# Performance work log

Hardware: AMD Instinct MI355X
Metric: run time of the kernel (lower is better)

Reference implementation:

```python
import jax, jax.numpy as jnp
import numpy as np

B, C, H, W, O = 32, 512, 28, 28, 1024


def _make_sketch(key, input_dim, output_dim):
    kh, ks = jax.random.split(key)
    rand_h = jax.random.randint(kh, (input_dim,), 0, output_dim)
    rand_s = jax.random.randint(ks, (input_dim,), 0, 2).astype(jnp.float32) * 2.0 - 1.0
    sketch = jnp.zeros((output_dim, input_dim), dtype=jnp.float32)
    return sketch.at[rand_h, jnp.arange(input_dim)].set(rand_s)


def setup_inputs() -> dict:
    key = jax.random.key(0)
    k1, k2, k3, k4 = jax.random.split(key, 4)
    x1 = jax.random.normal(k1, (B, C, H, W), dtype=jnp.float32)
    x2 = jax.random.normal(k2, (B, C, H, W), dtype=jnp.float32)
    sketch1 = _make_sketch(k3, C, O)
    sketch2 = _make_sketch(k4, C, O)
    return {"x1": x1, "x2": x2, "sketch1": sketch1, "sketch2": sketch2}


def reference(x1, x2, sketch1, sketch2):
    b, c, h, w = x1.shape
    out_dim = sketch1.shape[0]
    # [B, C, H*W] -> [B, N, C]
    x1_flat = x1.reshape(b, c, h * w).transpose(0, 2, 1)
    x2_flat = x2.reshape(b, c, h * w).transpose(0, 2, 1)
    # count-sketch projection via dense matmul (faithful to F.linear)
    proj1 = jnp.einsum('bnc,oc->bno', x1_flat, sketch1)
    proj2 = jnp.einsum('bnc,oc->bno', x2_flat, sketch2)
    orig_dtype = proj1.dtype
    # circular convolution via FFT along output_dim axis
    fft1 = jnp.fft.fft(proj1.astype(jnp.float32), axis=-1)
    fft2 = jnp.fft.fft(proj2.astype(jnp.float32), axis=-1)
    cbp_flat = jnp.fft.ifft(fft1 * fft2, axis=-1).real.astype(orig_dtype)
    # [B, N, O] -> [B, O, H, W]
    return cbp_flat.transpose(0, 2, 1).reshape(b, out_dim, h, w)
```

## Files before the change

kernel.cpp:

```cpp
#include <hip/hip_runtime.h>

#define O_DIM   1024
#define C_DIM   512
#define HW      784
#define B_DIM   32
#define T_POS   8
#define NTILES  (HW / T_POS)
#define NTHREADS 256

typedef float v2f __attribute__((ext_vector_type(2)));

__device__ __forceinline__ v2f cmul(v2f a, v2f b) {
    v2f bs = __builtin_shufflevector(b, b, 1, 0);
    v2f an = {-a.y, a.y};
    return a.x * b + an * bs;
}

static constexpr int REV5[32] = {
    0,16,8,24,4,20,12,28,2,18,10,26,6,22,14,30,
    1,17,9,25,5,21,13,29,3,19,11,27,7,23,15,31};

static constexpr float C32T[16] = {
    1.f, 0.98078528f, 0.92387953f, 0.83146961f,
    0.70710678f, 0.55557023f, 0.38268343f, 0.19509032f,
    0.f, -0.19509032f, -0.38268343f, -0.55557023f,
    -0.70710678f, -0.83146961f, -0.92387953f, -0.98078528f};
static constexpr float S32T[16] = {
    0.f, 0.19509032f, 0.38268343f, 0.55557023f,
    0.70710678f, 0.83146961f, 0.92387953f, 0.98078528f,
    1.f, 0.98078528f, 0.92387953f, 0.83146961f,
    0.70710678f, 0.55557023f, 0.38268343f, 0.19509032f};

__device__ __forceinline__ void fft32f(v2f y[32]) {
#pragma unroll
    for (int s = 0; s < 5; ++s) {
        const int L = 32 >> s;
        const int h = 16 >> s;
#pragma unroll
        for (int u = 0; u < 16; ++u) {
            const int blk = u >> (4 - s);
            const int t   = u & (h - 1);
            const int i   = blk * L + t;
            const int m   = t << s;
            v2f a = y[i], b = y[i + h];
            y[i] = a + b;
            v2f d = a - b;
            if (m == 0) {
                y[i + h] = d;
            } else if (m == 8) {
                y[i + h] = (v2f){d.y, -d.x};
            } else {
                y[i + h] = cmul(d, (v2f){C32T[m], -S32T[m]});
            }
        }
    }
}

__device__ __forceinline__ void four_step_Bf(v2f* zg, int p, v2f y[32]) {
    float sv, cv;
    __sincosf(-6.283185307179586f * (float)p * (1.f / 1024.f), &sv, &cv);
    const v2f stw = {cv, sv};
    v2f t2  = cmul(stw, stw);
    v2f t4  = cmul(t2, t2);
    v2f s8  = cmul(t4, t4);
    v2f s16 = cmul(s8, s8);
    v2f s24 = cmul(s16, s8);
    v2f wq0 = {1.f, 0.f}, wq1 = s8, wq2 = s16, wq3 = s24;
#pragma unroll
    for (int m = 0; m < 8; ++m) {
        {   const int k2 = m;
            v2f val = y[REV5[k2]];
            if (k2 > 0) val = cmul(val, wq0);
            zg[k2 * 32 + ((p + k2) & 31)] = val; }
        {   const int k2 = 8 + m;
            zg[k2 * 32 + ((p + k2) & 31)] = cmul(y[REV5[k2]], wq1); }
        {   const int k2 = 16 + m;
            zg[k2 * 32 + ((p + k2) & 31)] = cmul(y[REV5[k2]], wq2); }
        {   const int k2 = 24 + m;
            zg[k2 * 32 + ((p + k2) & 31)] = cmul(y[REV5[k2]], wq3); }
        if (m < 7) {
            wq0 = cmul(wq0, stw); wq1 = cmul(wq1, stw);
            wq2 = cmul(wq2, stw); wq3 = cmul(wq3, stw);
        }
    }
    __builtin_amdgcn_wave_barrier();
#pragma unroll
    for (int n1 = 0; n1 < 32; ++n1)
        y[n1] = zg[p * 32 + ((n1 + p) & 31)];
    __builtin_amdgcn_wave_barrier();
    fft32f(y);
}

__global__ void extract_sketch(const float* __restrict__ sk1,
                               const float* __restrict__ sk2,
                               int* __restrict__ h, float* __restrict__ s) {
    const int o = blockIdx.x;
    for (int c = threadIdx.x; c < C_DIM; c += blockDim.x) {
        float v1 = sk1[o * C_DIM + c];
        if (v1 != 0.f) { h[c] = o; s[c] = v1; }
        float v2 = sk2[o * C_DIM + c];
        if (v2 != 0.f) { h[C_DIM + c] = o; s[C_DIM + c] = v2; }
    }
}

__global__ __launch_bounds__(NTHREADS, 2)
void cbp_main(const float* __restrict__ x1, const float* __restrict__ x2,
              const int* __restrict__ h1, const int* __restrict__ h2,
              const float* __restrict__ s1, const float* __restrict__ s2,
              float* __restrict__ out) {
    __shared__ float4 LBUF[4096];
    float* Zs = reinterpret_cast<float*>(LBUF);
    float* R  = reinterpret_cast<float*>(LBUF);

    const int tid  = threadIdx.x;
    const int b    = blockIdx.x / NTILES;
    const int tile = blockIdx.x % NTILES;
    const int n0   = tile * T_POS;

    const int c0 = tid;
    const int c1 = tid + NTHREADS;
    const int xoff = b * (C_DIM * HW) + n0;
    const float4* p10 = (const float4*)(x1 + xoff + c0 * HW);
    const float4* p11 = (const float4*)(x1 + xoff + c1 * HW);
    const float4* p20 = (const float4*)(x2 + xoff + c0 * HW);
    const float4* p21 = (const float4*)(x2 + xoff + c1 * HW);
    float4 a0 = p10[0], a1 = p10[1];
    float4 b0 = p11[0], b1 = p11[1];
    float4 d0 = p20[0], d1 = p20[1];
    float4 e0 = p21[0], e1 = p21[1];
    const int   q10 = h1[c0], q11 = h1[c1], q20 = h2[c0], q21 = h2[c1];
    const float w10 = s1[c0], w11 = s1[c1], w20 = s2[c0], w21 = s2[c1];

#pragma unroll
    for (int i = 0; i < 4096 / NTHREADS; ++i)
        LBUF[tid + NTHREADS * i] = make_float4(0.f, 0.f, 0.f, 0.f);
    __syncthreads();

    {
        float v[8];
        v[0]=a0.x; v[1]=a0.y; v[2]=a0.z; v[3]=a0.w;
        v[4]=a1.x; v[5]=a1.y; v[6]=a1.z; v[7]=a1.w;
#pragma unroll
        for (int j = 0; j < 8; ++j)
            atomicAdd(&Zs[(j * O_DIM + q10) * 2 + 0], w10 * v[j]);
        v[0]=b0.x; v[1]=b0.y; v[2]=b0.z; v[3]=b0.w;
        v[4]=b1.x; v[5]=b1.y; v[6]=b1.z; v[7]=b1.w;
#pragma unroll
        for (int j = 0; j < 8; ++j)
            atomicAdd(&Zs[(j * O_DIM + q11) * 2 + 0], w11 * v[j]);
        v[0]=d0.x; v[1]=d0.y; v[2]=d0.z; v[3]=d0.w;
        v[4]=d1.x; v[5]=d1.y; v[6]=d1.z; v[7]=d1.w;
#pragma unroll
        for (int j = 0; j < 8; ++j)
            atomicAdd(&Zs[(j * O_DIM + q20) * 2 + 1], w20 * v[j]);
        v[0]=e0.x; v[1]=e0.y; v[2]=e0.z; v[3]=e0.w;
        v[4]=e1.x; v[5]=e1.y; v[6]=e1.z; v[7]=e1.w;
#pragma unroll
        for (int j = 0; j < 8; ++j)
            atomicAdd(&Zs[(j * O_DIM + q21) * 2 + 1], w21 * v[j]);
    }
    __syncthreads();

    const int g    = tid >> 5;
    const int p    = tid & 31;
    const int lane = tid & 63;
    v2f* zg = reinterpret_cast<v2f*>(LBUF) + g * O_DIM;
    const int paddr = (((lane & 32) | ((32 - p) & 31))) << 2;

    v2f y[32];

#pragma unroll 1
    for (int iter = 0; iter < 2; ++iter) {
        if (iter == 0) {
#pragma unroll
            for (int n2 = 0; n2 < 32; ++n2)
                y[n2] = zg[p + 32 * n2];
            __builtin_amdgcn_wave_barrier();
        } else {
            v2f t[32];
#pragma unroll
            for (int n2 = 0; n2 < 32; ++n2) {
                v2f za = y[REV5[n2]];
                v2f yb = y[REV5[31 - n2]];
                v2f zb;
                zb.x = __uint_as_float((unsigned)__builtin_amdgcn_ds_bpermute(
                           paddr, (int)__float_as_uint(yb.x)));
                zb.y = __uint_as_float((unsigned)__builtin_amdgcn_ds_bpermute(
                           paddr, (int)__float_as_uint(yb.y)));
                v2f self = y[REV5[(32 - n2) & 31]];
                zb.x = (p == 0) ? self.x : zb.x;
                zb.y = (p == 0) ? self.y : zb.y;
                v2f F1c = { za.x + zb.x, zb.y - za.y };
                v2f F2c = { za.y + zb.y, za.x - zb.x };
                t[n2] = cmul(F1c, F2c);
            }
#pragma unroll
            for (int i = 0; i < 32; ++i) y[i] = t[i];
        }
        fft32f(y);
        four_step_Bf(zg, p, y);
    }
    __syncthreads();

#pragma unroll
    for (int k1 = 0; k1 < 32; ++k1)
        R[(p + 32 * k1) * 10 + g] = y[REV5[k1]].x * (0.25f / 1024.f);
    __syncthreads();

    const int obase = b * (O_DIM * HW) + n0;
#pragma unroll
    for (int r = 0; r < O_DIM / NTHREADS; ++r) {
        const int o = tid + NTHREADS * r;
        const float* rp = &R[o * 10];
        float4 v0 = make_float4(rp[0], rp[1], rp[2], rp[3]);
        float4 v1 = make_float4(rp[4], rp[5], rp[6], rp[7]);
        float4* dst = (float4*)(out + obase + o * HW);
        dst[0] = v0;
        dst[1] = v1;
    }
}

extern "C" void kernel_launch(void* const* d_in, const int* in_sizes, int n_in,
                              void* d_out, int out_size, void* d_ws, size_t ws_size,
                              hipStream_t stream) {
    const float* x1  = (const float*)d_in[0];
    const float* x2  = (const float*)d_in[1];
    const float* sk1 = (const float*)d_in[2];
    const float* sk2 = (const float*)d_in[3];
    float* out = (float*)d_out;

    int*   h = (int*)d_ws;
    float* s = (float*)((char*)d_ws + 4096);

    hipLaunchKernelGGL(extract_sketch, dim3(O_DIM), dim3(256), 0, stream,
                       sk1, sk2, h, s);
    hipLaunchKernelGGL(cbp_main, dim3(B_DIM * NTILES), dim3(NTHREADS), 0, stream,
                       x1, x2, h, h + C_DIM, s, s + C_DIM, out);
}
```

Baseline: 359.6 us.

## Halve position tile per block, swizzle block-to-work mapping, use workgroup-scope LDS atomics

Each block now handles 4 spatial positions with 128 threads and half the LDS. That doubles the block count and should raise occupancy. Block IDs are remapped in a strided way, probably to spread neighbouring tiles across XCDs. The scatter atomics now use relaxed workgroup-scope fetch_add, and the output staging buffer uses a tighter pad. In exchange, each block writes only 16-byte segments per output row, which may hurt write coalescing, and each thread issues more x loads and atomics.

```diff
diff --git a/kernel.cpp b/kernel.cpp
--- a/kernel.cpp
+++ b/kernel.cpp
@@ -4,9 +4,11 @@
 #define C_DIM   512
 #define HW      784
 #define B_DIM   32
-#define T_POS   8
+#define T_POS   4
 #define NTILES  (HW / T_POS)
-#define NTHREADS 256
+#define NTHREADS 128
+#define NBLK    (B_DIM * NTILES)
+#define RPAD    5
 
 typedef float v2f __attribute__((ext_vector_type(2)));
 
@@ -108,56 +110,49 @@
               const int* __restrict__ h1, const int* __restrict__ h2,
               const float* __restrict__ s1, const float* __restrict__ s2,
               float* __restrict__ out) {
-    __shared__ float4 LBUF[4096];
+    __shared__ float4 LBUF[2048];
     float* Zs = reinterpret_cast<float*>(LBUF);
     float* R  = reinterpret_cast<float*>(LBUF);
 
-    const int tid  = threadIdx.x;
-    const int b    = blockIdx.x / NTILES;
-    const int tile = blockIdx.x % NTILES;
+    const int tid = threadIdx.x;
+    const int wid  = blockIdx.x;
+    const int work = (wid & 7) * (NBLK >> 3) + (wid >> 3);
+    const int b    = work / NTILES;
+    const int tile = work % NTILES;
     const int n0   = tile * T_POS;
 
-    const int c0 = tid;
-    const int c1 = tid + NTHREADS;
     const int xoff = b * (C_DIM * HW) + n0;
-    const float4* p10 = (const float4*)(x1 + xoff + c0 * HW);
-    const float4* p11 = (const float4*)(x1 + xoff + c1 * HW);
-    const float4* p20 = (const float4*)(x2 + xoff + c0 * HW);
-    const float4* p21 = (const float4*)(x2 + xoff + c1 * HW);
-    float4 a0 = p10[0], a1 = p10[1];
-    float4 b0 = p11[0], b1 = p11[1];
-    float4 d0 = p20[0], d1 = p20[1];
-    float4 e0 = p21[0], e1 = p21[1];
-    const int   q10 = h1[c0], q11 = h1[c1], q20 = h2[c0], q21 = h2[c1];
-    const float w10 = s1[c0], w11 = s1[c1], w20 = s2[c0], w21 = s2[c1];
-
-#pragma unroll
-    for (int i = 0; i < 4096 / NTHREADS; ++i)
+    float4 xa[4], xb[4];
+    int    qa[4], qb[4];
+    float  wa[4], wb[4];
+#pragma unroll
+    for (int r = 0; r < 4; ++r) {
+        const int c = tid + NTHREADS * r;
+        xa[r] = *(const float4*)(x1 + xoff + c * HW);
+        xb[r] = *(const float4*)(x2 + xoff + c * HW);
+        qa[r] = h1[c];  qb[r] = h2[c];
+        wa[r] = s1[c];  wb[r] = s2[c];
+    }
+
+#pragma unroll
+    for (int i = 0; i < 2048 / NTHREADS; ++i)
         LBUF[tid + NTHREADS * i] = make_float4(0.f, 0.f, 0.f, 0.f);
     __syncthreads();
 
-    {
-        float v[8];
-        v[0]=a0.x; v[1]=a0.y; v[2]=a0.z; v[3]=a0.w;
-        v[4]=a1.x; v[5]=a1.y; v[6]=a1.z; v[7]=a1.w;
-#pragma unroll
-        for (int j = 0; j < 8; ++j)
-            atomicAdd(&Zs[(j * O_DIM + q10) * 2 + 0], w10 * v[j]);
-        v[0]=b0.x; v[1]=b0.y; v[2]=b0.z; v[3]=b0.w;
-        v[4]=b1.x; v[5]=b1.y; v[6]=b1.z; v[7]=b1.w;
-#pragma unroll
-        for (int j = 0; j < 8; ++j)
-            atomicAdd(&Zs[(j * O_DIM + q11) * 2 + 0], w11 * v[j]);
-        v[0]=d0.x; v[1]=d0.y; v[2]=d0.z; v[3]=d0.w;
-        v[4]=d1.x; v[5]=d1.y; v[6]=d1.z; v[7]=d1.w;
-#pragma unroll
-        for (int j = 0; j < 8; ++j)
-            atomicAdd(&Zs[(j * O_DIM + q20) * 2 + 1], w20 * v[j]);
-        v[0]=e0.x; v[1]=e0.y; v[2]=e0.z; v[3]=e0.w;
-        v[4]=e1.x; v[5]=e1.y; v[6]=e1.z; v[7]=e1.w;
-#pragma unroll
-        for (int j = 0; j < 8; ++j)
-            atomicAdd(&Zs[(j * O_DIM + q21) * 2 + 1], w21 * v[j]);
+#pragma unroll
+    for (int r = 0; r < 4; ++r) {
+        float va[4] = {xa[r].x, xa[r].y, xa[r].z, xa[r].w};
+#pragma unroll
+        for (int j = 0; j < 4; ++j)
+            __hip_atomic_fetch_add(&Zs[(j * O_DIM + qa[r]) * 2 + 0],
+                                   wa[r] * va[j],
+                                   __ATOMIC_RELAXED, __HIP_MEMORY_SCOPE_WORKGROUP);
+        float vb[4] = {xb[r].x, xb[r].y, xb[r].z, xb[r].w};
+#pragma unroll
+        for (int j = 0; j < 4; ++j)
+            __hip_atomic_fetch_add(&Zs[(j * O_DIM + qb[r]) * 2 + 1],
+                                   wb[r] * vb[j],
+                                   __ATOMIC_RELAXED, __HIP_MEMORY_SCOPE_WORKGROUP);
     }
     __syncthreads();
 
@@ -204,19 +199,16 @@
 
 #pragma unroll
     for (int k1 = 0; k1 < 32; ++k1)
-        R[(p + 32 * k1) * 10 + g] = y[REV5[k1]].x * (0.25f / 1024.f);
+        R[(p + 32 * k1) * RPAD + g] = y[REV5[k1]].x * (0.25f / 1024.f);
     __syncthreads();
 
     const int obase = b * (O_DIM * HW) + n0;
 #pragma unroll
     for (int r = 0; r < O_DIM / NTHREADS; ++r) {
         const int o = tid + NTHREADS * r;
-        const float* rp = &R[o * 10];
+        const float* rp = &R[o * RPAD];
         float4 v0 = make_float4(rp[0], rp[1], rp[2], rp[3]);
-        float4 v1 = make_float4(rp[4], rp[5], rp[6], rp[7]);
-        float4* dst = (float4*)(out + obase + o * HW);
-        dst[0] = v0;
-        dst[1] = v1;
+        *(float4*)(out + obase + o * HW) = v0;
     }
 }
 
@@ -234,6 +226,6 @@
 
     hipLaunchKernelGGL(extract_sketch, dim3(O_DIM), dim3(256), 0, stream,
                        sk1, sk2, h, s);
-    hipLaunchKernelGGL(cbp_main, dim3(B_DIM * NTILES), dim3(NTHREADS), 0, stream,
+    hipLaunchKernelGGL(cbp_main, dim3(NBLK), dim3(NTHREADS), 0, stream,
                        x1, x2, h, h + C_DIM, s, s + C_DIM, out);
 }
```

New measurement: 353.6 us. About the same (-1.7%).
